# Kernel optimization log

Hardware: AMD Instinct MI355X
Metric: run time of the kernel (lower is better)

Reference implementation:

```python
import jax, jax.numpy as jnp
import numpy as np

N = 10000
K1, K2 = 10, 25
DIM = 64
OUT = 128
NUM_GRAPHS = 64


def setup_inputs() -> dict:
    key = jax.random.key(0)
    ks = jax.random.split(key, 10)
    h0 = jax.random.normal(ks[0], (N, DIM), jnp.float32)
    h1 = jax.random.normal(ks[1], (N * K1, DIM), jnp.float32)
    h2 = jax.random.normal(ks[2], (N * K1 * K2, DIM), jnp.float32)
    # glorot-ish scaled weights
    w0 = jax.random.normal(ks[3], (2 * DIM, OUT), jnp.float32) * (2.0 / (2 * DIM + OUT)) ** 0.5
    b0 = jnp.zeros((OUT,), jnp.float32)
    w1 = jax.random.normal(ks[4], (2 * OUT, OUT), jnp.float32) * (2.0 / (3 * OUT)) ** 0.5
    b1 = jnp.zeros((OUT,), jnp.float32)
    wr1 = jax.random.normal(ks[5], (OUT, 35), jnp.float32) * (2.0 / (OUT + 35)) ** 0.5
    br1 = jnp.zeros((35,), jnp.float32)
    wr2 = jax.random.normal(ks[6], (35, 35), jnp.float32) * (2.0 / 70) ** 0.5
    br2 = jnp.zeros((35,), jnp.float32)
    wr3 = jax.random.normal(ks[7], (35, 1), jnp.float32) * (2.0 / 36) ** 0.5
    br3 = jnp.zeros((1,), jnp.float32)
    states_graph_ids = jnp.sort(jax.random.randint(ks[8], (N,), 0, NUM_GRAPHS, jnp.int32))
    return {
        "h0": h0, "h1": h1, "h2": h2,
        "w0": w0, "b0": b0, "w1": w1, "b1": b1,
        "wr1": wr1, "br1": br1, "wr2": wr2, "br2": br2, "wr3": wr3, "br3": br3,
        "states_graph_ids": states_graph_ids, "num_graphs": NUM_GRAPHS,
    }


def _aggr_mean(src, neigh, w, b):
    # GraphSAGE mean aggregator: concat(src, mean(neighbors)) @ w + b, relu
    n, d = src.shape
    k = neigh.shape[0] // n
    neigh_mean = neigh.reshape(n, k, d).mean(axis=1)  # (n, d)
    return jax.nn.relu(jnp.concatenate([src, neigh_mean], axis=1) @ w + b)


def reference(h0, h1, h2, w0, b0, w1, b1, wr1, br1, wr2, br2, wr3, br3,
              states_graph_ids, num_graphs):
    # round 0: shared aggregator across depths
    a01 = _aggr_mean(h0, h1, w0, b0)          # (N, OUT)
    a12 = _aggr_mean(h1, h2, w0, b0)          # (N*K1, OUT)
    # round 1
    out = _aggr_mean(a01, a12, w1, b1)        # (N, OUT)
    # segment_sum over sorted graph ids
    seg = jax.ops.segment_sum(out, states_graph_ids, num_segments=num_graphs,
                              indices_are_sorted=True)  # (G, OUT)
    # readout MLP (dropout inactive at inference)
    r = jax.nn.selu(seg @ wr1 + br1)
    r = jax.nn.selu(r @ wr2 + br2)
    r = r @ wr3 + br3                          # (G, 1)
    return r
```

## Files before the change

kernel.cpp:

```cpp
#include <hip/hip_runtime.h>
#include <hip/hip_bf16.h>
#include <math.h>

#define N_NODES 10000
#define K1 10
#define K2 25
#define DIM 64
#define OUT 128
#define NGRAPH 64

__global__ __launch_bounds__(256, 4) void kA(const float* __restrict__ h1,
                                             const float* __restrict__ h2,
                                             const float* __restrict__ w0,
                                             const float* __restrict__ b0,
                                             float* __restrict__ a12mean)
{
    __shared__ float  xbuf[K1][2 * DIM];
    __shared__ float4 red4[16][16];
    __shared__ float  pbuf[K1][OUT];

    const int t    = threadIdx.x;
    const int node = blockIdx.x;
    const int c    = t & 127;
    const int h    = t >> 7;

    float w0r[64];
#pragma unroll
    for (int k = 0; k < 64; ++k)
        w0r[k] = w0[(h * 64 + k) * OUT + c];
    const float b0r = b0[c];

    {
        const float* h1b = h1 + (size_t)node * (K1 * DIM);
        for (int idx = t; idx < K1 * DIM; idx += 256)
            xbuf[idx >> 6][idx & 63] = h1b[idx];
    }

    const int cc = t & 15;
    const int sl = t >> 4;
    const float4* h2b = (const float4*)h2 + (size_t)node * (K1 * K2 * DIM / 4);
    for (int j = 0; j < K1; ++j) {
        const float4* bj = h2b + j * (K2 * DIM / 4);
        float4 s = bj[sl * 16 + cc];
        if (sl < 9) {
            float4 s2 = bj[(sl + 16) * 16 + cc];
            s.x += s2.x; s.y += s2.y; s.z += s2.z; s.w += s2.w;
        }
        red4[sl][cc] = s;
        __syncthreads();
        if (t < 64) {
            const float* rf = (const float*)red4;
            float sum = 0.f;
#pragma unroll
            for (int ss = 0; ss < 16; ++ss) sum += rf[ss * 64 + t];
            xbuf[j][DIM + t] = sum * (1.0f / K2);
        }
        __syncthreads();
    }

    float myp[K1];
#pragma unroll
    for (int j = 0; j < K1; ++j) {
        const float4* xj = (const float4*)(&xbuf[j][h * DIM]);
        float p = 0.f;
#pragma unroll
        for (int k4 = 0; k4 < 16; ++k4) {
            float4 xv = xj[k4];
            p += xv.x * w0r[4 * k4 + 0];
            p += xv.y * w0r[4 * k4 + 1];
            p += xv.z * w0r[4 * k4 + 2];
            p += xv.w * w0r[4 * k4 + 3];
        }
        if (h == 1) pbuf[j][c] = p;
        else        myp[j]     = p;
    }
    __syncthreads();
    if (h == 0) {
        float acc = 0.f;
#pragma unroll
        for (int j = 0; j < K1; ++j) {
            float y = myp[j] + pbuf[j][c] + b0r;
            acc += (y > 0.f ? y : 0.f);
        }
        a12mean[(size_t)node * OUT + c] = acc * (1.0f / K1);
    }
}

__global__ __launch_bounds__(256, 2) void kB(const float* __restrict__ h0,
                                             const float* __restrict__ h1,
                                             const float* __restrict__ w0,
                                             const float* __restrict__ b0,
                                             const float* __restrict__ w1,
                                             const float* __restrict__ b1,
                                             const float* __restrict__ a12mean,
                                             const int*   __restrict__ gids,
                                             float* __restrict__ seg)
{
    __shared__ float x0[16][2 * DIM];
    __shared__ float x1[16][2 * OUT];
    __shared__ float pbuf[16][OUT];

    const int t  = threadIdx.x;
    const int n0 = blockIdx.x * 16;
    const int c  = t & 127;
    const int hh = t >> 7;

    float w0r[64];
#pragma unroll
    for (int k = 0; k < 64; ++k)
        w0r[k] = w0[(hh * 64 + k) * OUT + c];
    const float b0r = b0[c];

    for (int idx = t; idx < 16 * DIM; idx += 256)
        x0[idx >> 6][idx & 63] = h0[(size_t)n0 * DIM + idx];

    {
        const int col = t & 63, isub = t >> 6;
        for (int chunk = 0; chunk < 4; ++chunk) {
            const int il = chunk * 4 + isub;
            const float* b = h1 + (size_t)(n0 + il) * (K1 * DIM);
            float s = 0.f;
#pragma unroll
            for (int r = 0; r < K1; ++r) s += b[r * DIM + col];
            x0[il][DIM + col] = s * (1.0f / K1);
        }
    }

    for (int idx = t; idx < 16 * OUT; idx += 256)
        x1[idx >> 7][OUT + (idx & 127)] = a12mean[(size_t)n0 * OUT + idx];
    __syncthreads();

    float myp[16];
#pragma unroll
    for (int i = 0; i < 16; ++i) {
        const float4* xi = (const float4*)(&x0[i][hh * DIM]);
        float p = 0.f;
#pragma unroll
        for (int k4 = 0; k4 < 16; ++k4) {
            float4 xv = xi[k4];
            p += xv.x * w0r[4 * k4 + 0] + xv.y * w0r[4 * k4 + 1]
               + xv.z * w0r[4 * k4 + 2] + xv.w * w0r[4 * k4 + 3];
        }
        if (hh == 1) pbuf[i][c] = p; else myp[i] = p;
    }
    __syncthreads();
    if (hh == 0) {
#pragma unroll
        for (int i = 0; i < 16; ++i) {
            float y = myp[i] + pbuf[i][c] + b0r;
            x1[i][c] = (y > 0.f ? y : 0.f);
        }
    }

    float w1r[128];
#pragma unroll
    for (int k = 0; k < 128; ++k)
        w1r[k] = w1[(hh * 128 + k) * OUT + c];
    const float b1r = b1[c];
    __syncthreads();

#pragma unroll
    for (int i = 0; i < 16; ++i) {
        const float4* xi = (const float4*)(&x1[i][hh * OUT]);
        float p = 0.f;
#pragma unroll
        for (int k4 = 0; k4 < 32; ++k4) {
            float4 xv = xi[k4];
            p += xv.x * w1r[4 * k4 + 0] + xv.y * w1r[4 * k4 + 1]
               + xv.z * w1r[4 * k4 + 2] + xv.w * w1r[4 * k4 + 3];
        }
        if (hh == 1) pbuf[i][c] = p; else myp[i] = p;
    }
    __syncthreads();
    if (hh == 0) {
        int   runGid = gids[n0];
        float runSum = 0.f;
#pragma unroll
        for (int i = 0; i < 16; ++i) {
            float y = myp[i] + pbuf[i][c] + b1r;
            y = (y > 0.f ? y : 0.f);
            const int g = gids[n0 + i];
            if (g != runGid) {
                atomicAdd(&seg[runGid * OUT + c], runSum);
                runSum = 0.f; runGid = g;
            }
            runSum += y;
        }
        atomicAdd(&seg[runGid * OUT + c], runSum);
    }
}

__global__ void kC(const float* __restrict__ seg,
                   const float* __restrict__ wr1, const float* __restrict__ br1,
                   const float* __restrict__ wr2, const float* __restrict__ br2,
                   const float* __restrict__ wr3, const float* __restrict__ br3,
                   float* __restrict__ out)
{
    __shared__ float r1[35], r2[35];
    const int g = blockIdx.x, l = threadIdx.x;
    const float* s = seg + (size_t)g * OUT;
    const float SCALE = 1.0507009873554805f;
    const float ALPHA = 1.6732632423543772f;

    if (l < 35) {
        float d = br1[l];
        for (int k = 0; k < OUT; ++k) d += s[k] * wr1[k * 35 + l];
        r1[l] = d > 0.f ? SCALE * d : SCALE * ALPHA * (expf(d) - 1.f);
    }
    __syncthreads();
    if (l < 35) {
        float d = br2[l];
        for (int k = 0; k < 35; ++k) d += r1[k] * wr2[k * 35 + l];
        r2[l] = d > 0.f ? SCALE * d : SCALE * ALPHA * (expf(d) - 1.f);
    }
    __syncthreads();
    if (l == 0) {
        float d = br3[0];
        for (int k = 0; k < 35; ++k) d += r2[k] * wr3[k];
        out[g] = d;
    }
}

extern "C" void kernel_launch(void* const* d_in, const int* in_sizes, int n_in,
                              void* d_out, int out_size, void* d_ws, size_t ws_size,
                              hipStream_t stream)
{
    const float* h0  = (const float*)d_in[0];
    const float* h1  = (const float*)d_in[1];
    const float* h2  = (const float*)d_in[2];
    const float* w0  = (const float*)d_in[3];
    const float* b0  = (const float*)d_in[4];
    const float* w1  = (const float*)d_in[5];
    const float* b1  = (const float*)d_in[6];
    const float* wr1 = (const float*)d_in[7];
    const float* br1 = (const float*)d_in[8];
    const float* wr2 = (const float*)d_in[9];
    const float* br2 = (const float*)d_in[10];
    const float* wr3 = (const float*)d_in[11];
    const float* br3 = (const float*)d_in[12];
    const int*  gids = (const int*)d_in[13];

    float* a12mean = (float*)d_ws;
    float* seg     = a12mean + (size_t)N_NODES * OUT;
    float* out     = (float*)d_out;

    hipMemsetAsync(seg, 0, NGRAPH * OUT * sizeof(float), stream);
    kA<<<N_NODES, 256, 0, stream>>>(h1, h2, w0, b0, a12mean);
    kB<<<N_NODES / 16, 256, 0, stream>>>(h0, h1, w0, b0, w1, b1, a12mean, gids, seg);
    kC<<<NGRAPH, 64, 0, stream>>>(seg, wr1, br1, wr2, br2, wr3, br3, out);
}
```

Measured before the change: 920.5 us.

## Split h2 neighbor mean into streaming kernel and widen kB to 512 threads

```diff
diff --git a/kernel.cpp b/kernel.cpp
--- a/kernel.cpp
+++ b/kernel.cpp
@@ -9,15 +9,32 @@
 #define OUT 128
 #define NGRAPH 64
 
-__global__ __launch_bounds__(256, 4) void kA(const float* __restrict__ h1,
-                                             const float* __restrict__ h2,
-                                             const float* __restrict__ w0,
-                                             const float* __restrict__ b0,
-                                             float* __restrict__ a12mean)
-{
-    __shared__ float  xbuf[K1][2 * DIM];
-    __shared__ float4 red4[16][16];
-    __shared__ float  pbuf[K1][OUT];
+__global__ __launch_bounds__(256) void kMean(const float4* __restrict__ h2,
+                                             float4* __restrict__ h2mean)
+{
+    const int u   = blockIdx.x * 256 + threadIdx.x;
+    const int row = u >> 4;
+    const int c4  = u & 15;
+    const float4* p = h2 + (size_t)row * (K2 * DIM / 4) + c4;
+    float4 s = make_float4(0.f, 0.f, 0.f, 0.f);
+#pragma unroll
+    for (int k = 0; k < K2; ++k) {
+        float4 v = p[k * (DIM / 4)];
+        s.x += v.x; s.y += v.y; s.z += v.z; s.w += v.w;
+    }
+    const float inv = 1.0f / K2;
+    s.x *= inv; s.y *= inv; s.z *= inv; s.w *= inv;
+    h2mean[u] = s;
+}
+
+__global__ __launch_bounds__(256, 4) void kA2(const float* __restrict__ h1,
+                                              const float* __restrict__ h2mean,
+                                              const float* __restrict__ w0,
+                                              const float* __restrict__ b0,
+                                              float* __restrict__ a12mean)
+{
+    __shared__ float xbuf[K1][2 * DIM];
+    __shared__ float pbuf[K1][OUT];
 
     const int t    = threadIdx.x;
     const int node = blockIdx.x;
@@ -31,32 +48,15 @@
     const float b0r = b0[c];
 
     {
-        const float* h1b = h1 + (size_t)node * (K1 * DIM);
-        for (int idx = t; idx < K1 * DIM; idx += 256)
-            xbuf[idx >> 6][idx & 63] = h1b[idx];
-    }
-
-    const int cc = t & 15;
-    const int sl = t >> 4;
-    const float4* h2b = (const float4*)h2 + (size_t)node * (K1 * K2 * DIM / 4);
-    for (int j = 0; j < K1; ++j) {
-        const float4* bj = h2b + j * (K2 * DIM / 4);
-        float4 s = bj[sl * 16 + cc];
-        if (sl < 9) {
-            float4 s2 = bj[(sl + 16) * 16 + cc];
-            s.x += s2.x; s.y += s2.y; s.z += s2.z; s.w += s2.w;
-        }
-        red4[sl][cc] = s;
-        __syncthreads();
-        if (t < 64) {
-            const float* rf = (const float*)red4;
-            float sum = 0.f;
-#pragma unroll
-            for (int ss = 0; ss < 16; ++ss) sum += rf[ss * 64 + t];
-            xbuf[j][DIM + t] = sum * (1.0f / K2);
-        }
-        __syncthreads();
-    }
+        const float4* h1b = (const float4*)(h1 + (size_t)node * (K1 * DIM));
+        const float4* mb  = (const float4*)(h2mean + (size_t)node * (K1 * DIM));
+        for (int idx = t; idx < K1 * DIM / 4; idx += 256) {
+            const int j = idx >> 4, cc = idx & 15;
+            ((float4*)&xbuf[j][0])[cc]   = h1b[idx];
+            ((float4*)&xbuf[j][DIM])[cc] = mb[idx];
+        }
+    }
+    __syncthreads();
 
     float myp[K1];
 #pragma unroll
@@ -66,10 +66,8 @@
 #pragma unroll
         for (int k4 = 0; k4 < 16; ++k4) {
             float4 xv = xj[k4];
-            p += xv.x * w0r[4 * k4 + 0];
-            p += xv.y * w0r[4 * k4 + 1];
-            p += xv.z * w0r[4 * k4 + 2];
-            p += xv.w * w0r[4 * k4 + 3];
+            p += xv.x * w0r[4 * k4 + 0] + xv.y * w0r[4 * k4 + 1]
+               + xv.z * w0r[4 * k4 + 2] + xv.w * w0r[4 * k4 + 3];
         }
         if (h == 1) pbuf[j][c] = p;
         else        myp[j]     = p;
@@ -86,7 +84,7 @@
     }
 }
 
-__global__ __launch_bounds__(256, 2) void kB(const float* __restrict__ h0,
+__global__ __launch_bounds__(512, 2) void kB(const float* __restrict__ h0,
                                              const float* __restrict__ h1,
                                              const float* __restrict__ w0,
                                              const float* __restrict__ b0,
@@ -98,86 +96,88 @@
 {
     __shared__ float x0[16][2 * DIM];
     __shared__ float x1[16][2 * OUT];
-    __shared__ float pbuf[16][OUT];
+    __shared__ float pq[4][16][OUT];
 
     const int t  = threadIdx.x;
     const int n0 = blockIdx.x * 16;
     const int c  = t & 127;
-    const int hh = t >> 7;
-
-    float w0r[64];
+    const int q  = t >> 7;
+
+    float w0q[32];
+#pragma unroll
+    for (int k = 0; k < 32; ++k)
+        w0q[k] = w0[(q * 32 + k) * OUT + c];
+
+    for (int idx = t; idx < 16 * DIM; idx += 512)
+        x0[idx >> 6][idx & 63] = h0[(size_t)n0 * DIM + idx];
+
+    {
+        const int col = t & 63, i0 = t >> 6;
+#pragma unroll
+        for (int rep = 0; rep < 2; ++rep) {
+            const int i = i0 + rep * 8;
+            const float* b = h1 + (size_t)(n0 + i) * (K1 * DIM);
+            float s = 0.f;
+#pragma unroll
+            for (int r = 0; r < K1; ++r) s += b[r * DIM + col];
+            x0[i][DIM + col] = s * (1.0f / K1);
+        }
+    }
+
+    for (int idx = t; idx < 16 * OUT; idx += 512)
+        x1[idx >> 7][OUT + (idx & 127)] = a12mean[(size_t)n0 * OUT + idx];
+    __syncthreads();
+
+#pragma unroll
+    for (int i = 0; i < 16; ++i) {
+        const float4* xi = (const float4*)&x0[i][q * 32];
+        float p = 0.f;
+#pragma unroll
+        for (int k4 = 0; k4 < 8; ++k4) {
+            float4 v = xi[k4];
+            p += v.x * w0q[4 * k4 + 0] + v.y * w0q[4 * k4 + 1]
+               + v.z * w0q[4 * k4 + 2] + v.w * w0q[4 * k4 + 3];
+        }
+        pq[q][i][c] = p;
+    }
+
+    float w1q[64];
 #pragma unroll
     for (int k = 0; k < 64; ++k)
-        w0r[k] = w0[(hh * 64 + k) * OUT + c];
-    const float b0r = b0[c];
-
-    for (int idx = t; idx < 16 * DIM; idx += 256)
-        x0[idx >> 6][idx & 63] = h0[(size_t)n0 * DIM + idx];
-
-    {
-        const int col = t & 63, isub = t >> 6;
-        for (int chunk = 0; chunk < 4; ++chunk) {
-            const int il = chunk * 4 + isub;
-            const float* b = h1 + (size_t)(n0 + il) * (K1 * DIM);
-            float s = 0.f;
-#pragma unroll
-            for (int r = 0; r < K1; ++r) s += b[r * DIM + col];
-            x0[il][DIM + col] = s * (1.0f / K1);
-        }
-    }
-
-    for (int idx = t; idx < 16 * OUT; idx += 256)
-        x1[idx >> 7][OUT + (idx & 127)] = a12mean[(size_t)n0 * OUT + idx];
-    __syncthreads();
-
-    float myp[16];
+        w1q[k] = w1[(q * 64 + k) * OUT + c];
+    __syncthreads();
+
+    if (q == 0) {
+        const float b0r = b0[c];
+#pragma unroll
+        for (int i = 0; i < 16; ++i) {
+            float y = pq[0][i][c] + pq[1][i][c] + pq[2][i][c] + pq[3][i][c] + b0r;
+            x1[i][c] = (y > 0.f ? y : 0.f);
+        }
+    }
+    __syncthreads();
+
 #pragma unroll
     for (int i = 0; i < 16; ++i) {
-        const float4* xi = (const float4*)(&x0[i][hh * DIM]);
+        const float4* xi = (const float4*)&x1[i][q * 64];
         float p = 0.f;
 #pragma unroll
         for (int k4 = 0; k4 < 16; ++k4) {
-            float4 xv = xi[k4];
-            p += xv.x * w0r[4 * k4 + 0] + xv.y * w0r[4 * k4 + 1]
-               + xv.z * w0r[4 * k4 + 2] + xv.w * w0r[4 * k4 + 3];
-        }
-        if (hh == 1) pbuf[i][c] = p; else myp[i] = p;
-    }
-    __syncthreads();
-    if (hh == 0) {
-#pragma unroll
-        for (int i = 0; i < 16; ++i) {
-            float y = myp[i] + pbuf[i][c] + b0r;
-            x1[i][c] = (y > 0.f ? y : 0.f);
-        }
-    }
-
-    float w1r[128];
-#pragma unroll
-    for (int k = 0; k < 128; ++k)
-        w1r[k] = w1[(hh * 128 + k) * OUT + c];
-    const float b1r = b1[c];
-    __syncthreads();
-
-#pragma unroll
-    for (int i = 0; i < 16; ++i) {
-        const float4* xi = (const float4*)(&x1[i][hh * OUT]);
-        float p = 0.f;
-#pragma unroll
-        for (int k4 = 0; k4 < 32; ++k4) {
-            float4 xv = xi[k4];
-            p += xv.x * w1r[4 * k4 + 0] + xv.y * w1r[4 * k4 + 1]
-               + xv.z * w1r[4 * k4 + 2] + xv.w * w1r[4 * k4 + 3];
-        }
-        if (hh == 1) pbuf[i][c] = p; else myp[i] = p;
-    }
-    __syncthreads();
-    if (hh == 0) {
+            float4 v = xi[k4];
+            p += v.x * w1q[4 * k4 + 0] + v.y * w1q[4 * k4 + 1]
+               + v.z * w1q[4 * k4 + 2] + v.w * w1q[4 * k4 + 3];
+        }
+        pq[q][i][c] = p;
+    }
+    __syncthreads();
+
+    if (q == 0) {
+        const float b1r = b1[c];
         int   runGid = gids[n0];
         float runSum = 0.f;
 #pragma unroll
         for (int i = 0; i < 16; ++i) {
-            float y = myp[i] + pbuf[i][c] + b1r;
+            float y = pq[0][i][c] + pq[1][i][c] + pq[2][i][c] + pq[3][i][c] + b1r;
             y = (y > 0.f ? y : 0.f);
             const int g = gids[n0 + i];
             if (g != runGid) {
@@ -242,10 +242,13 @@
 
     float* a12mean = (float*)d_ws;
     float* seg     = a12mean + (size_t)N_NODES * OUT;
+    float* h2mean  = seg + (size_t)NGRAPH * OUT;
     float* out     = (float*)d_out;
 
     hipMemsetAsync(seg, 0, NGRAPH * OUT * sizeof(float), stream);
-    kA<<<N_NODES, 256, 0, stream>>>(h1, h2, w0, b0, a12mean);
-    kB<<<N_NODES / 16, 256, 0, stream>>>(h0, h1, w0, b0, w1, b1, a12mean, gids, seg);
+    kMean<<<(N_NODES * K1 * (DIM / 4)) / 256, 256, 0, stream>>>(
+        (const float4*)h2, (float4*)h2mean);
+    kA2<<<N_NODES, 256, 0, stream>>>(h1, h2mean, w0, b0, a12mean);
+    kB<<<N_NODES / 16, 512, 0, stream>>>(h0, h1, w0, b0, w1, b1, a12mean, gids, seg);
     kC<<<NGRAPH, 64, 0, stream>>>(seg, wr1, br1, wr2, br2, wr3, br3, out);
 }
```

Result: slower. 954.0 us (+3.6%).
